# Kernel optimization log

Measured on AMD Instinct MI355X. Metric: run time of the kernel, lower is better.

## Reference

```python
import jax, jax.numpy as jnp
import numpy as np

BLOCK_SIZE = 16
E2M1_LOOKUP = jnp.array([0.0, 0.5, 1.0, 1.5, 2.0, 3.0, 4.0, 6.0], dtype=jnp.float32)


def setup_inputs() -> dict:
    key = jax.random.key(0)
    k1, k2, k3, k4, k5 = jax.random.split(key, 5)
    in_features, out_features = 8192, 8192
    x = jax.random.normal(k1, (64, in_features), dtype=jnp.float32)
    weight_packed = jax.random.randint(k2, (out_features, in_features // 2), 0, 256, dtype=jnp.int32)
    weight_scale = jax.random.uniform(k3, (out_features, in_features // BLOCK_SIZE), dtype=jnp.float32)
    weight_global_scale = jax.random.uniform(k4, (1,), dtype=jnp.float32) + 0.5
    bias = jax.random.normal(k5, (out_features,), dtype=jnp.float32)
    return {"x": x, "weight_packed": weight_packed, "weight_scale": weight_scale,
            "weight_global_scale": weight_global_scale, "bias": bias}


def unpack_nvfp4(weight_packed, weight_scale, weight_global_scale, dtype=jnp.float32):
    out_features, in_packed = weight_packed.shape
    in_features = in_packed * 2
    low = weight_packed & 15
    high = (weight_packed >> 4) & 15
    # per-byte order: low nibble first, then high nibble
    combined = jnp.stack([low, high], axis=-1).reshape(out_features, in_features)
    signs = (combined >> 3) & 1
    mag_idx = combined & 7
    values = E2M1_LOOKUP[mag_idx] * (1.0 - 2.0 * signs.astype(jnp.float32))
    # per-block (16-wide) scale
    values = (values.reshape(out_features, -1, BLOCK_SIZE) * weight_scale[..., None]).reshape(out_features, in_features)
    g = weight_global_scale.reshape(())
    actual_scale = jnp.where(g != 0, 1.0 / g, 1.0)
    return (values * actual_scale).astype(dtype)


def reference(x, weight_packed, weight_scale, weight_global_scale, bias):
    W = unpack_nvfp4(weight_packed, weight_scale, weight_global_scale, dtype=x.dtype)
    return x @ W.T + bias
```

## Files before the change

kernel.cpp:

```cpp
#include <hip/hip_runtime.h>
#include <stdint.h>

typedef _Float16 f16x2 __attribute__((ext_vector_type(2)));
typedef _Float16 f16x8 __attribute__((ext_vector_type(8)));
typedef float f32x4 __attribute__((ext_vector_type(4)));

static __device__ __forceinline__ uint32_t perm(uint32_t hi, uint32_t lo, uint32_t sel) {
    return __builtin_amdgcn_perm(hi, lo, sel);
}
static __device__ __forceinline__ f16x2 bch2(uint32_t u) { union { uint32_t x; f16x2 h; } c; c.x = u; return c.h; }
static __device__ __forceinline__ uint32_t bcu(f16x2 h) { union { uint32_t x; f16x2 h; } c; c.h = h; return c.x; }
static __device__ __forceinline__ uint32_t pkrtz(float a, float b) {
    auto r = __builtin_amdgcn_cvt_pkrtz(a, b);
    union { decltype(r) h; uint32_t u; } c; c.h = r; return c.u;
}

#define NTOT 8192
#define KTOT 8192
#define SPLITS 16
#define KCHUNK 512
#define BN 256

__global__ __launch_bounds__(256, 2) void nvfp4_init_out(const float* __restrict__ bias,
                                                         float* __restrict__ out) {
    int i = blockIdx.x * 256 + threadIdx.x;
    ((f32x4*)out)[i] = ((const f32x4*)bias)[i & 2047];
}

__global__ __launch_bounds__(256, 2) void nvfp4_gemm(const float* __restrict__ x,
                                                     const int* __restrict__ wp,
                                                     const float* __restrict__ ws,
                                                     const float* __restrict__ gs,
                                                     float* __restrict__ out) {
    __shared__ __align__(16) uint8_t xl[64 * 256 * 2];
    __shared__ float sl[256 * 33];

    const int tid = threadIdx.x;
    const int nb = blockIdx.x & 31;
    const int ksp = blockIdx.x >> 5;
    const int nbase = nb * BN;
    const int kc0 = ksp * KCHUNK;

    {
        float g = gs[0];
        float inv_g = (g != 0.0f) ? (1.0f / g) : 1.0f;
        int r = tid >> 3;
        int c = (tid & 7) * 4;
        for (int p = 0; p < 8; ++p) {
            int row = r + p * 32;
            f32x4 v = *(const f32x4*)(ws + (size_t)(nbase + row) * 512 + (kc0 >> 4) + c);
            sl[row * 33 + c + 0] = v.x * inv_g;
            sl[row * 33 + c + 1] = v.y * inv_g;
            sl[row * 33 + c + 2] = v.z * inv_g;
            sl[row * 33 + c + 3] = v.w * inv_g;
        }
    }

    const int lane = tid & 63;
    const int wid = tid >> 6;
    const int l15 = lane & 15;
    const int grp = lane >> 4;

    f32x4 acc[4][4];
    #pragma unroll
    for (int a = 0; a < 4; ++a)
        #pragma unroll
        for (int b = 0; b < 4; ++b)
            acc[a][b] = f32x4{0.f, 0.f, 0.f, 0.f};

    const uint32_t TH = 0x46444240u, TL = 0x3E3C3800u;

    for (int half = 0; half < 2; ++half) {
        __syncthreads();
        {
            int a = tid >> 5;
            int b = tid & 31;
            int cb = b * 8;
            const float* xp = x + (size_t)a * KTOT + kc0 + half * 256 + cb;
            #pragma unroll
            for (int j = 0; j < 8; ++j) {
                int row = a + j * 8;
                f32x4 v0 = *(const f32x4*)(xp + (size_t)j * 8 * KTOT);
                f32x4 v1 = *(const f32x4*)(xp + (size_t)j * 8 * KTOT + 4);
                uint4 d;
                d.x = pkrtz(v0.x, v0.y);
                d.y = pkrtz(v0.z, v0.w);
                d.z = pkrtz(v1.x, v1.y);
                d.w = pkrtz(v1.z, v1.w);
                uint32_t addr = ((uint32_t)(row * 512 + cb * 2)) ^ ((row & 7) << 4);
                *(uint4*)(xl + addr) = d;
            }
        }
        __syncthreads();

        #pragma unroll 2
        for (int kk = 0; kk < 8; ++kk) {
            const int kg = kc0 + half * 256 + kk * 32;
            int4 w4[4];
            float sf[4];
            const int scol = half * 16 + kk * 2 + (grp >> 1);
            #pragma unroll
            for (int ss = 0; ss < 4; ++ss) {
                int wrow = nbase + wid * 64 + ss * 16 + l15;
                w4[ss] = *(const int4*)(wp + (size_t)wrow * 4096 + (kg >> 1) + grp * 4);
                sf[ss] = sl[(wid * 64 + ss * 16 + l15) * 33 + scol];
            }
            f16x8 af[4];
            #pragma unroll
            for (int mt = 0; mt < 4; ++mt) {
                int row = mt * 16 + l15;
                uint32_t addr = ((uint32_t)(row * 512 + (kk * 32 + grp * 8) * 2)) ^ ((row & 7) << 4);
                af[mt] = *(const f16x8*)(xl + addr);
            }
            #pragma unroll
            for (int ss = 0; ss < 4; ++ss) {
                f16x2 s2 = bch2(pkrtz(sf[ss], sf[ss]));
                uint32_t b = (uint32_t)(w4[ss].x & 0xff) | ((uint32_t)(w4[ss].y & 0xff) << 8) |
                             ((uint32_t)(w4[ss].z & 0xff) << 16) | ((uint32_t)w4[ss].w << 24);
                uint32_t sel_e = b & 0x07070707u;
                uint32_t sel_o = (b >> 4) & 0x07070707u;
                uint32_t he = perm(TH, TL, sel_e) | ((b & 0x08080808u) << 4);
                uint32_t ho = perm(TH, TL, sel_o) | (b & 0x80808080u);
                uint32_t d0 = perm(ho, he, 0x040C000Cu);
                uint32_t d1 = perm(ho, he, 0x050C010Cu);
                uint32_t d2 = perm(ho, he, 0x060C020Cu);
                uint32_t d3 = perm(ho, he, 0x070C030Cu);
                union { uint32_t u[4]; f16x8 h; } fr;
                fr.u[0] = bcu(bch2(d0) * s2);
                fr.u[1] = bcu(bch2(d1) * s2);
                fr.u[2] = bcu(bch2(d2) * s2);
                fr.u[3] = bcu(bch2(d3) * s2);
                #pragma unroll
                for (int mt = 0; mt < 4; ++mt)
                    acc[mt][ss] = __builtin_amdgcn_mfma_f32_16x16x32_f16(af[mt], fr.h, acc[mt][ss], 0, 0, 0);
            }
        }
    }

    #pragma unroll
    for (int mt = 0; mt < 4; ++mt)
        #pragma unroll
        for (int ss = 0; ss < 4; ++ss)
            #pragma unroll
            for (int q = 0; q < 4; ++q) {
                int row = mt * 16 + grp * 4 + q;
                int col = nbase + wid * 64 + ss * 16 + l15;
                unsafeAtomicAdd(out + (size_t)row * NTOT + col, acc[mt][ss][q]);
            }
}

extern "C" void kernel_launch(void* const* d_in, const int* in_sizes, int n_in,
                              void* d_out, int out_size, void* d_ws, size_t ws_size,
                              hipStream_t stream) {
    const float* x = (const float*)d_in[0];
    const int* wp = (const int*)d_in[1];
    const float* ws = (const float*)d_in[2];
    const float* gs = (const float*)d_in[3];
    const float* bias = (const float*)d_in[4];
    float* out = (float*)d_out;

    nvfp4_init_out<<<dim3(512), dim3(256), 0, stream>>>(bias, out);
    nvfp4_gemm<<<dim3(SPLITS * (NTOT / BN)), dim3(256), 0, stream>>>(x, wp, ws, gs, out);
}
```

Before: 230.8 us.

## Double workgroup size to 8 waves and prefetch next weight chunk

The GEMM workgroup grows from 256 to 512 threads, so each of the 8 waves covers 32 output columns instead of 64, halving per-wave accumulators and weight loads. The K loop is fully unrolled and software-pipelined: the next int4 weight fragment is loaded from global memory while the current one is dequantized and fed to MFMA. Block scales are stored pre-converted to packed fp16 pairs in LDS, which removes a per-use conversion. Launch bounds now request 4 blocks of 512 threads, which tightens the register budget, and LDS use (about 66 KB per block) may cap occupancy below that target.

```diff
diff --git a/kernel.cpp b/kernel.cpp
--- a/kernel.cpp
+++ b/kernel.cpp
@@ -27,13 +27,13 @@
     ((f32x4*)out)[i] = ((const f32x4*)bias)[i & 2047];
 }
 
-__global__ __launch_bounds__(256, 2) void nvfp4_gemm(const float* __restrict__ x,
+__global__ __launch_bounds__(512, 4) void nvfp4_gemm(const float* __restrict__ x,
                                                      const int* __restrict__ wp,
                                                      const float* __restrict__ ws,
                                                      const float* __restrict__ gs,
                                                      float* __restrict__ out) {
     __shared__ __align__(16) uint8_t xl[64 * 256 * 2];
-    __shared__ float sl[256 * 33];
+    __shared__ uint32_t sl[256 * 33];
 
     const int tid = threadIdx.x;
     const int nb = blockIdx.x & 31;
@@ -44,15 +44,18 @@
     {
         float g = gs[0];
         float inv_g = (g != 0.0f) ? (1.0f / g) : 1.0f;
-        int r = tid >> 3;
-        int c = (tid & 7) * 4;
-        for (int p = 0; p < 8; ++p) {
-            int row = r + p * 32;
-            f32x4 v = *(const f32x4*)(ws + (size_t)(nbase + row) * 512 + (kc0 >> 4) + c);
-            sl[row * 33 + c + 0] = v.x * inv_g;
-            sl[row * 33 + c + 1] = v.y * inv_g;
-            sl[row * 33 + c + 2] = v.z * inv_g;
-            sl[row * 33 + c + 3] = v.w * inv_g;
+        int row = tid >> 1;
+        int cb = (tid & 1) * 16;
+        const f32x4* sp = (const f32x4*)(ws + (size_t)(nbase + row) * 512 + (kc0 >> 4) + cb);
+        uint32_t* d = sl + row * 33 + cb;
+        #pragma unroll
+        for (int q = 0; q < 4; ++q) {
+            f32x4 v = sp[q];
+            float a0 = v.x * inv_g, a1 = v.y * inv_g, a2 = v.z * inv_g, a3 = v.w * inv_g;
+            d[q * 4 + 0] = pkrtz(a0, a0);
+            d[q * 4 + 1] = pkrtz(a1, a1);
+            d[q * 4 + 2] = pkrtz(a2, a2);
+            d[q * 4 + 3] = pkrtz(a3, a3);
         }
     }
 
@@ -61,90 +64,103 @@
     const int l15 = lane & 15;
     const int grp = lane >> 4;
 
-    f32x4 acc[4][4];
+    auto stage_x = [&](int h) {
+        int a = tid >> 5;
+        int cb8 = (tid & 31) * 8;
+        const float* xp = x + (size_t)a * KTOT + kc0 + h * 256 + cb8;
+        #pragma unroll
+        for (int j = 0; j < 4; ++j) {
+            int row = a + j * 16;
+            f32x4 v0 = *(const f32x4*)(xp + (size_t)j * 16 * KTOT);
+            f32x4 v1 = *(const f32x4*)(xp + (size_t)j * 16 * KTOT + 4);
+            uint4 d;
+            d.x = pkrtz(v0.x, v0.y);
+            d.y = pkrtz(v0.z, v0.w);
+            d.z = pkrtz(v1.x, v1.y);
+            d.w = pkrtz(v1.z, v1.w);
+            uint32_t addr = ((uint32_t)(row * 512 + cb8 * 2)) ^ ((row & 7) << 4);
+            *(uint4*)(xl + addr) = d;
+        }
+    };
+
+    f32x4 acc[4][2];
     #pragma unroll
     for (int a = 0; a < 4; ++a)
         #pragma unroll
-        for (int b = 0; b < 4; ++b)
+        for (int b = 0; b < 2; ++b)
             acc[a][b] = f32x4{0.f, 0.f, 0.f, 0.f};
 
     const uint32_t TH = 0x46444240u, TL = 0x3E3C3800u;
 
-    for (int half = 0; half < 2; ++half) {
-        __syncthreads();
-        {
-            int a = tid >> 5;
-            int b = tid & 31;
-            int cb = b * 8;
-            const float* xp = x + (size_t)a * KTOT + kc0 + half * 256 + cb;
+    const int wrow0 = nbase + wid * 32 + l15;
+    const int* wp0 = wp + (size_t)wrow0 * 4096 + (kc0 >> 1) + grp * 4;
+    const int* wp1 = wp + (size_t)(wrow0 + 16) * 4096 + (kc0 >> 1) + grp * 4;
+    const int srow0 = (wid * 32 + l15) * 33;
+    const int srow1 = (wid * 32 + 16 + l15) * 33;
+
+    stage_x(0);
+    int4 wc0 = *(const int4*)(wp0);
+    int4 wc1 = *(const int4*)(wp1);
+    __syncthreads();
+
+    #pragma unroll
+    for (int t = 0; t < 16; ++t) {
+        if (t == 8) {
+            __syncthreads();
+            stage_x(1);
+            __syncthreads();
+        }
+        int4 wn0, wn1;
+        if (t < 15) {
+            wn0 = *(const int4*)(wp0 + (t + 1) * 16);
+            wn1 = *(const int4*)(wp1 + (t + 1) * 16);
+        }
+        f16x8 af[4];
+        #pragma unroll
+        for (int mt = 0; mt < 4; ++mt) {
+            int row = mt * 16 + l15;
+            uint32_t addr = ((uint32_t)(row * 512 + ((t & 7) * 32 + grp * 8) * 2)) ^ ((row & 7) << 4);
+            af[mt] = *(const f16x8*)(xl + addr);
+        }
+        const int scol = t * 2 + (grp >> 1);
+        f16x2 s2a = bch2(sl[srow0 + scol]);
+        f16x2 s2b = bch2(sl[srow1 + scol]);
+
+        #pragma unroll
+        for (int ss = 0; ss < 2; ++ss) {
+            const int4 w4 = ss ? wc1 : wc0;
+            const f16x2 s2 = ss ? s2b : s2a;
+            uint32_t b = (uint32_t)(w4.x & 0xff) | ((uint32_t)(w4.y & 0xff) << 8) |
+                         ((uint32_t)(w4.z & 0xff) << 16) | ((uint32_t)w4.w << 24);
+            uint32_t sel_e = b & 0x07070707u;
+            uint32_t sel_o = (b >> 4) & 0x07070707u;
+            uint32_t he = perm(TH, TL, sel_e) | ((b & 0x08080808u) << 4);
+            uint32_t ho = perm(TH, TL, sel_o) | (b & 0x80808080u);
+            uint32_t d0 = perm(ho, he, 0x040C000Cu);
+            uint32_t d1 = perm(ho, he, 0x050C010Cu);
+            uint32_t d2 = perm(ho, he, 0x060C020Cu);
+            uint32_t d3 = perm(ho, he, 0x070C030Cu);
+            union { uint32_t u[4]; f16x8 h; } fr;
+            fr.u[0] = bcu(bch2(d0) * s2);
+            fr.u[1] = bcu(bch2(d1) * s2);
+            fr.u[2] = bcu(bch2(d2) * s2);
+            fr.u[3] = bcu(bch2(d3) * s2);
             #pragma unroll
-            for (int j = 0; j < 8; ++j) {
-                int row = a + j * 8;
-                f32x4 v0 = *(const f32x4*)(xp + (size_t)j * 8 * KTOT);
-                f32x4 v1 = *(const f32x4*)(xp + (size_t)j * 8 * KTOT + 4);
-                uint4 d;
-                d.x = pkrtz(v0.x, v0.y);
-                d.y = pkrtz(v0.z, v0.w);
-                d.z = pkrtz(v1.x, v1.y);
-                d.w = pkrtz(v1.z, v1.w);
-                uint32_t addr = ((uint32_t)(row * 512 + cb * 2)) ^ ((row & 7) << 4);
-                *(uint4*)(xl + addr) = d;
-            }
+            for (int mt = 0; mt < 4; ++mt)
+                acc[mt][ss] = __builtin_amdgcn_mfma_f32_16x16x32_f16(af[mt], fr.h, acc[mt][ss], 0, 0, 0);
         }
-        __syncthreads();
-
-        #pragma unroll 2
-        for (int kk = 0; kk < 8; ++kk) {
-            const int kg = kc0 + half * 256 + kk * 32;
-            int4 w4[4];
-            float sf[4];
-            const int scol = half * 16 + kk * 2 + (grp >> 1);
-            #pragma unroll
-            for (int ss = 0; ss < 4; ++ss) {
-                int wrow = nbase + wid * 64 + ss * 16 + l15;
-                w4[ss] = *(const int4*)(wp + (size_t)wrow * 4096 + (kg >> 1) + grp * 4);
-                sf[ss] = sl[(wid * 64 + ss * 16 + l15) * 33 + scol];
-            }
-            f16x8 af[4];
-            #pragma unroll
-            for (int mt = 0; mt < 4; ++mt) {
-                int row = mt * 16 + l15;
-                uint32_t addr = ((uint32_t)(row * 512 + (kk * 32 + grp * 8) * 2)) ^ ((row & 7) << 4);
-                af[mt] = *(const f16x8*)(xl + addr);
-            }
-            #pragma unroll
-            for (int ss = 0; ss < 4; ++ss) {
-                f16x2 s2 = bch2(pkrtz(sf[ss], sf[ss]));
-                uint32_t b = (uint32_t)(w4[ss].x & 0xff) | ((uint32_t)(w4[ss].y & 0xff) << 8) |
-                             ((uint32_t)(w4[ss].z & 0xff) << 16) | ((uint32_t)w4[ss].w << 24);
-                uint32_t sel_e = b & 0x07070707u;
-                uint32_t sel_o = (b >> 4) & 0x07070707u;
-                uint32_t he = perm(TH, TL, sel_e) | ((b & 0x08080808u) << 4);
-                uint32_t ho = perm(TH, TL, sel_o) | (b & 0x80808080u);
-                uint32_t d0 = perm(ho, he, 0x040C000Cu);
-                uint32_t d1 = perm(ho, he, 0x050C010Cu);
-                uint32_t d2 = perm(ho, he, 0x060C020Cu);
-                uint32_t d3 = perm(ho, he, 0x070C030Cu);
-                union { uint32_t u[4]; f16x8 h; } fr;
-                fr.u[0] = bcu(bch2(d0) * s2);
-                fr.u[1] = bcu(bch2(d1) * s2);
-                fr.u[2] = bcu(bch2(d2) * s2);
-                fr.u[3] = bcu(bch2(d3) * s2);
-                #pragma unroll
-                for (int mt = 0; mt < 4; ++mt)
-                    acc[mt][ss] = __builtin_amdgcn_mfma_f32_16x16x32_f16(af[mt], fr.h, acc[mt][ss], 0, 0, 0);
-            }
-        }
+        wc0 = wn0;
+        wc1 = wn1;
     }
 
     #pragma unroll
     for (int mt = 0; mt < 4; ++mt)
         #pragma unroll
-        for (int ss = 0; ss < 4; ++ss)
+        for (int ss = 0; ss < 2; ++ss)
             #pragma unroll
             for (int q = 0; q < 4; ++q) {
                 int row = mt * 16 + grp * 4 + q;
-                int col = nbase + wid * 64 + ss * 16 + l15;
+                int col = nbase + wid * 32 + ss * 16 + l15;
                 unsafeAtomicAdd(out + (size_t)row * NTOT + col, acc[mt][ss][q]);
             }
 }
@@ -160,5 +176,5 @@
     float* out = (float*)d_out;
 
     nvfp4_init_out<<<dim3(512), dim3(256), 0, stream>>>(bias, out);
-    nvfp4_gemm<<<dim3(SPLITS * (NTOT / BN)), dim3(256), 0, stream>>>(x, wp, ws, gs, out);
+    nvfp4_gemm<<<dim3(SPLITS * (NTOT / BN)), dim3(512), 0, stream>>>(x, wp, ws, gs, out);
 }
```

After: 235.7 us. +2.1%, slower.
